# Optimization experiments

Measured on AMD Instinct MI355X. Metric: run time of the kernel, lower is better.

Reference implementation:

```python
import jax, jax.numpy as jnp
import numpy as np

B, S, D, H = 2, 2048, 1024, 16
DH = D // H
EPS = 1e-5


def setup_inputs() -> dict:
    key = jax.random.key(0)
    ks = jax.random.split(key, 12)
    inp = {
        "Q_source": jax.random.normal(ks[0], (B, S, D), jnp.float32),
        "K_source": jax.random.normal(ks[1], (B, S, D), jnp.float32),
        "V_source": jax.random.normal(ks[2], (B, S, D), jnp.float32),
        "padding_mask": jnp.zeros((B, 1, 1, S), dtype=bool),  # no padded keys (avoids NaN rows)
        "future_mask": jnp.triu(jnp.ones((S, S), dtype=bool), k=1)[None, None],  # causal
    }
    sc = 1.0 / np.sqrt(D)
    names = ["WQ", "WK", "WV", "WO"]
    for i, n in enumerate(names):
        inp[n] = jax.random.normal(ks[3 + i], (D, D), jnp.float32) * sc
        inp["b" + n[1]] = jnp.zeros((D,), jnp.float32)
    inp["gamma"] = jnp.ones((D,), jnp.float32)
    inp["beta"] = jnp.zeros((D,), jnp.float32)
    return inp


def reference(Q_source, K_source, V_source, padding_mask, future_mask,
              WQ, bQ, WK, bK, WV, bV, WO, bO, gamma, beta):
    b = Q_source.shape[0]
    # torch Linear: x @ W.T + b ; reshape to [B, H, S, DH]
    def proj(x, W, bb):
        y = x @ W.T + bb
        return y.reshape(b, -1, H, DH).transpose(0, 2, 1, 3)

    Q = proj(Q_source, WQ, bQ)
    K = proj(K_source, WK, bK)
    V = proj(V_source, WV, bV)

    scores = jnp.einsum("bhqd,bhkd->bhqk", Q, K) / jnp.sqrt(jnp.float32(DH))
    neg_inf = jnp.float32(-jnp.inf)
    scores = jnp.where(padding_mask, neg_inf, scores)
    scores = jnp.where(future_mask, neg_inf, scores)
    attn = jax.nn.softmax(scores, axis=-1)

    ctx = jnp.einsum("bhqk,bhkd->bhqd", attn, V)
    ctx = ctx.transpose(0, 2, 1, 3).reshape(b, -1, D)
    out = ctx @ WO.T + bO

    x = Q_source + out
    mu = x.mean(-1, keepdims=True)
    var = x.var(-1, keepdims=True)
    return (x - mu) * jax.lax.rsqrt(var + EPS) * gamma + beta
```

## Files before the change

### kernel.cpp

```cpp
#include <hip/hip_runtime.h>

#define S_LEN 2048
#define DMODEL 1024
#define NH 16
#define DHD 64

typedef __attribute__((ext_vector_type(8))) short bh8;
typedef __attribute__((ext_vector_type(4))) float f32x4;
typedef __attribute__((ext_vector_type(2))) unsigned int u32x2;
typedef __attribute__((ext_vector_type(4))) unsigned int u32x4;
typedef unsigned short u16;
typedef unsigned int u32;

static __device__ __forceinline__ u16 f2bf(float f) {
    unsigned u = __builtin_bit_cast(unsigned, f);
    u += 0x7fffu + ((u >> 16) & 1u);
    return (u16)(u >> 16);
}

typedef const __attribute__((address_space(1))) void* gptr_t;
typedef __attribute__((address_space(3))) void* lptr_t;

static __device__ __forceinline__ void gll16(const void* g, void* l) {
    __builtin_amdgcn_global_load_lds((gptr_t)g, (lptr_t)l, 16, 0, 0);
}

__global__ __launch_bounds__(256) void cvt_all(const float* __restrict__ WQ, const float* __restrict__ WK,
                                               const float* __restrict__ WV, const float* __restrict__ WO,
                                               const float* __restrict__ S0, const float* __restrict__ S1,
                                               const float* __restrict__ S2,
                                               u16* __restrict__ wq, u16* __restrict__ wk,
                                               u16* __restrict__ wv, u16* __restrict__ wo,
                                               u16* __restrict__ q0, u16* __restrict__ k0,
                                               u16* __restrict__ v0) {
    int bid = blockIdx.x;
    const float* s;
    u16* o;
    size_t base;
    if (bid < 2048) {
        int wi = bid >> 9;
        s = wi == 0 ? WQ : (wi == 1 ? WK : (wi == 2 ? WV : WO));
        o = wi == 0 ? wq : (wi == 1 ? wk : (wi == 2 ? wv : wo));
        base = (size_t)(bid & 511) * 2048;
    } else {
        int r = bid - 2048;
        int si = r >> 11;
        s = si == 0 ? S0 : (si == 1 ? S1 : S2);
        o = si == 0 ? q0 : (si == 1 ? k0 : v0);
        base = (size_t)(r & 2047) * 2048;
    }
    size_t i = base + (size_t)threadIdx.x * 8;
    float4 a = *(const float4*)(s + i);
    float4 b = *(const float4*)(s + i + 4);
    u32 p0 = (u32)f2bf(a.x) | ((u32)f2bf(a.y) << 16);
    u32 p1 = (u32)f2bf(a.z) | ((u32)f2bf(a.w) << 16);
    u32 p2 = (u32)f2bf(b.x) | ((u32)f2bf(b.y) << 16);
    u32 p3 = (u32)f2bf(b.z) | ((u32)f2bf(b.w) << 16);
    *(u32x4*)(o + i) = (u32x4){p0, p1, p2, p3};
}

template <int BM, int OBF, int AF32>
static __device__ __forceinline__ void gemm_body(const void* __restrict__ Ap, const u16* __restrict__ Bm,
                                                 const float* __restrict__ bias, void* __restrict__ Cv,
                                                 int N, int K, int bi, int bj, short* Al, short* Bl,
                                                 float oscale) {
    constexpr int MI = BM / 32;
    constexpr int NC = BM / 64;
    int tid = threadIdx.x, lane = tid & 63, w = tid >> 6;
    int ln = lane & 15, hi = lane >> 4;
    int wm = w >> 1, wn = w & 1;
    f32x4 acc[MI][4];
#pragma unroll
    for (int i = 0; i < MI; i++)
#pragma unroll
        for (int j = 0; j < 4; j++) acc[i][j] = (f32x4){0.f, 0.f, 0.f, 0.f};
    int nk = K >> 5;

    float4 fa[NC][2];
    auto loadA = [&](int kt) {
#pragma unroll
        for (int c = 0; c < NC; ++c) {
            int o = c * 4096 + tid * 16;
            int row = o >> 6, e0 = (o & 63) >> 1;
            const float* src = (const float*)Ap + (size_t)(bi * BM + row) * K + kt * 32 + e0;
            fa[c][0] = *(const float4*)src;
            fa[c][1] = *(const float4*)(src + 4);
        }
    };
    auto writeA = [&](int buf) {
#pragma unroll
        for (int c = 0; c < NC; ++c) {
            int o = c * 4096 + tid * 16;
            u32 w0 = (u32)f2bf(fa[c][0].x) | ((u32)f2bf(fa[c][0].y) << 16);
            u32 w1 = (u32)f2bf(fa[c][0].z) | ((u32)f2bf(fa[c][0].w) << 16);
            u32 w2 = (u32)f2bf(fa[c][1].x) | ((u32)f2bf(fa[c][1].y) << 16);
            u32 w3 = (u32)f2bf(fa[c][1].z) | ((u32)f2bf(fa[c][1].w) << 16);
            *(u32x4*)((char*)(Al + buf * (BM * 32)) + o) = (u32x4){w0, w1, w2, w3};
        }
    };
    auto stageA_lds = [&](int buf, int kt) {
#pragma unroll
        for (int c = 0; c < NC; ++c) {
            int o = c * 4096 + tid * 16;
            int row = o >> 6, col = (o & 63) >> 1;
            gll16((const u16*)Ap + (size_t)(bi * BM + row) * K + kt * 32 + col,
                  (char*)(Al + buf * (BM * 32)) + o);
        }
    };
    auto stageB = [&](int buf, int kt) {
#pragma unroll
        for (int c = 0; c < 2; ++c) {
            int o = c * 4096 + tid * 16;
            int row = o >> 6, col = (o & 63) >> 1;
            gll16(Bm + (size_t)(bj * 128 + row) * K + kt * 32 + col, (char*)(Bl + buf * 4096) + o);
        }
    };

    if constexpr (AF32) { loadA(0); writeA(0); } else { stageA_lds(0, 0); }
    stageB(0, 0);
    __syncthreads();
    int cur = 0;
    for (int kt = 0; kt < nk; ++kt) {
        bool pre = (kt + 1 < nk);
        if (pre) {
            if constexpr (AF32) loadA(kt + 1); else stageA_lds(cur ^ 1, kt + 1);
            stageB(cur ^ 1, kt + 1);
        }
        bh8 av[MI], bv[4];
#pragma unroll
        for (int i = 0; i < MI; i++) av[i] = *(const bh8*)&Al[cur * (BM * 32) + (wm * (BM / 2) + i * 16 + ln) * 32 + hi * 8];
#pragma unroll
        for (int j = 0; j < 4; j++) bv[j] = *(const bh8*)&Bl[cur * 4096 + (wn * 64 + j * 16 + ln) * 32 + hi * 8];
#pragma unroll
        for (int i = 0; i < MI; i++)
#pragma unroll
            for (int j = 0; j < 4; j++)
                acc[i][j] = __builtin_amdgcn_mfma_f32_16x16x32_bf16(av[i], bv[j], acc[i][j], 0, 0, 0);
        if constexpr (AF32) { if (pre) writeA(cur ^ 1); }
        __syncthreads();
        cur ^= 1;
    }
    if constexpr (OBF == 2) {
#pragma unroll
        for (int j = 0; j < 4; j++) {
            int col = wn * 64 + j * 16 + ln;
            float bvs = bias[bj * 128 + col];
#pragma unroll
            for (int i = 0; i < MI; i++) {
                int row0 = wm * (BM / 2) + i * 16 + hi * 4;
                u32 p01 = (u32)f2bf(acc[i][j][0] + bvs) | ((u32)f2bf(acc[i][j][1] + bvs) << 16);
                u32 p23 = (u32)f2bf(acc[i][j][2] + bvs) | ((u32)f2bf(acc[i][j][3] + bvs) << 16);
                int idx = col * 128 + (row0 ^ ((col & 7) << 3));
                *(u32x2*)&Al[idx] = (u32x2){p01, p23};
            }
        }
        __syncthreads();
        int b = bi >> 4;
        int sbase = (bi & 15) * 128;
#pragma unroll
        for (int it = 0; it < 8; ++it) {
            int idx = it * 256 + tid;
            int dcol = idx >> 4;
            int sl = (idx & 15) * 8;
            bh8 v = *(const bh8*)&Al[dcol * 128 + (sl ^ ((dcol & 7) << 3))];
            int h = bj * 2 + (dcol >> 6), d = dcol & 63;
            *(bh8*)((u16*)Cv + ((size_t)((b * 16 + h) * 64 + d)) * 2048 + sbase + sl) = v;
        }
        return;
    }
#pragma unroll
    for (int j = 0; j < 4; j++) {
        int col = bj * 128 + wn * 64 + j * 16 + ln;
        float bvs = bias[col];
#pragma unroll
        for (int i = 0; i < MI; i++) {
            int row0 = bi * BM + wm * (BM / 2) + i * 16 + hi * 4;
#pragma unroll
            for (int rr = 0; rr < 4; rr++) {
                if (OBF) {
                    float v = (acc[i][j][rr] + bvs) * oscale;
                    ((u16*)Cv)[(size_t)(row0 + rr) * N + col] = f2bf(v);
                } else {
                    ((float*)Cv)[(size_t)(row0 + rr) * N + col] = acc[i][j][rr] + bvs;
                }
            }
        }
    }
}

__global__ __launch_bounds__(256, 3) void gemm_qkv(const u16* __restrict__ A0, const u16* __restrict__ A1,
                                                   const u16* __restrict__ A2, const u16* __restrict__ B0,
                                                   const u16* __restrict__ B1, const u16* __restrict__ B2,
                                                   const float* __restrict__ c0, const float* __restrict__ c1,
                                                   const float* __restrict__ c2, u16* __restrict__ C0,
                                                   u16* __restrict__ C1, u16* __restrict__ VT) {
    __shared__ short SH[16384];
    short* Al = SH;
    short* Bl = SH + 8192;
    int bid = blockIdx.x;
    int swz = (bid & 7) * 96 + (bid >> 3);
    int z = swz >> 8, t = swz & 255;
    if (z == 2) {
        gemm_body<128, 2, 0>(A2, B2, c2, VT, 1024, 1024, t >> 3, t & 7, Al, Bl, 1.0f);
    } else if (z == 0) {
        gemm_body<128, 1, 0>(A0, B0, c0, C0, 1024, 1024, t >> 3, t & 7, Al, Bl, 0.18033688f);
    } else {
        gemm_body<128, 1, 0>(A1, B1, c1, C1, 1024, 1024, t >> 3, t & 7, Al, Bl, 1.0f);
    }
}

__global__ __launch_bounds__(256) void gemm_o(const u16* __restrict__ A, const u16* __restrict__ Bm,
                                              const float* __restrict__ bias, float* __restrict__ C) {
    __shared__ short Al[2 * 64 * 32];
    __shared__ short Bl[2 * 128 * 32];
    int bid = blockIdx.x;
    int swz = (bid & 7) * 64 + (bid >> 3);
    gemm_body<64, 0, 0>(A, Bm, bias, C, 1024, 1024, swz >> 3, swz & 7, Al, Bl, 1.0f);
}

template <int PLO, int PHI>
static __device__ __forceinline__ void attn_core(const u16* __restrict__ Qp, const u16* __restrict__ Kp,
                                                 const u16* __restrict__ VT, u16* __restrict__ Ctx,
                                                 short* Klb, short* Vlb, short* Pw, float* Csh, float* Lsh,
                                                 int b, int h, int bh, int qt, int tid) {
    int lane = tid & 63, w = tid >> 6;
    int grp = w >> 2;
    int qsub = w & 3;
    int tgl = tid & 255;
    int ln = lane & 15, hi = lane >> 4;
    __builtin_amdgcn_s_setprio(PLO);

    auto stage_kv = [&](int buf, int kt) {
#pragma unroll
        for (int c = 0; c < 2; ++c) {
            int o = c * 4096 + tgl * 16;
            int rr = o >> 7;
            int slot = (o >> 4) & 7;
            gll16(Kp + ((size_t)(b * S_LEN + kt * 64 + rr)) * DMODEL + h * DHD + ((slot ^ (rr & 7)) << 3),
                  (char*)(Klb + buf * 4096) + o);
            gll16(VT + ((size_t)(bh * DHD + rr)) * S_LEN + kt * 64 + ((slot ^ (rr & 7)) << 3),
                  (char*)(Vlb + buf * 4096) + o);
        }
    };

    int nh = qt + 1;
    int nt = 2 * qt + 2;
    int kbase = grp * nh;
    int qg0 = (qt << 7) + qsub * 32 + ln;
    const bh8* qr0 = (const bh8*)(Qp + ((size_t)(b * S_LEN + qg0)) * DMODEL + h * DHD);
    const bh8* qr1 = (const bh8*)(Qp + ((size_t)(b * S_LEN + qg0 + 16)) * DMODEL + h * DHD);
    bh8 qf[2][2];
    qf[0][0] = qr0[hi]; qf[0][1] = qr0[4 + hi];
    qf[1][0] = qr1[hi]; qf[1][1] = qr1[4 + hi];
    f32x4 ctxa[2][4];
    float ls[2] = {0.f, 0.f};
#pragma unroll
    for (int g = 0; g < 2; g++)
#pragma unroll
        for (int i = 0; i < 4; i++) ctxa[g][i] = (f32x4){0.f, 0.f, 0.f, 0.f};
    stage_kv(0, kbase);
    __syncthreads();
    int cur = 0;
    for (int i = 0; i < nh; ++i) {
        int kt = kbase + i;
        if (i + 1 < nh) stage_kv(cur ^ 1, kt + 1);
        f32x4 sc[2][4];
#pragma unroll
        for (int g = 0; g < 2; g++)
#pragma unroll
            for (int ks = 0; ks < 4; ++ks) sc[g][ks] = (f32x4){0.f, 0.f, 0.f, 0.f};
        __builtin_amdgcn_s_setprio(PHI);
#pragma unroll
        for (int dwin = 0; dwin < 2; ++dwin) {
#pragma unroll
            for (int ks = 0; ks < 4; ++ks) {
                int rr = ks * 16 + ln;
                bh8 kv = *(const bh8*)&Klb[cur * 4096 + rr * 64 + ((dwin * 32 + hi * 8) ^ ((rr & 7) << 3))];
                sc[0][ks] = __builtin_amdgcn_mfma_f32_16x16x32_bf16(kv, qf[0][dwin], sc[0][ks], 0, 0, 0);
                sc[1][ks] = __builtin_amdgcn_mfma_f32_16x16x32_bf16(kv, qf[1][dwin], sc[1][ks], 0, 0, 0);
            }
        }
        __builtin_amdgcn_s_setprio(PLO);
        if (kt >= nt - 2) {
#pragma unroll
            for (int g = 0; g < 2; g++) {
                int qgq = qg0 + g * 16;
#pragma unroll
                for (int ks = 0; ks < 4; ++ks)
#pragma unroll
                    for (int rr = 0; rr < 4; ++rr) {
                        int kg = kt * 64 + ks * 16 + hi * 4 + rr;
                        sc[g][ks][rr] = (kg <= qgq) ? sc[g][ks][rr] : -1e30f;
                    }
            }
        }
#pragma unroll
        for (int g = 0; g < 2; g++) {
#pragma unroll
            for (int ks = 0; ks < 4; ++ks) {
                float p0 = __builtin_amdgcn_exp2f(sc[g][ks][0]);
                float p1 = __builtin_amdgcn_exp2f(sc[g][ks][1]);
                float p2 = __builtin_amdgcn_exp2f(sc[g][ks][2]);
                float p3 = __builtin_amdgcn_exp2f(sc[g][ks][3]);
                ls[g] += (p0 + p1) + (p2 + p3);
                u32 u0 = __builtin_bit_cast(u32, p0);
                u32 u1 = __builtin_bit_cast(u32, p1);
                u32 u2 = __builtin_bit_cast(u32, p2);
                u32 u3 = __builtin_bit_cast(u32, p3);
                u32 a01 = (u0 >> 16) | (u1 & 0xffff0000u);
                u32 a23 = (u2 >> 16) | (u3 & 0xffff0000u);
                int kloc = ks * 16 + hi * 4;
                *(u32x2*)&Pw[ln * 64 + (kloc ^ ((ln & 7) << 3))] = (u32x2){a01, a23};
            }
            __builtin_amdgcn_s_setprio(PHI);
#pragma unroll
            for (int kw = 0; kw < 2; ++kw) {
                bh8 pf = *(const bh8*)&Pw[ln * 64 + ((kw * 32 + hi * 8) ^ ((ln & 7) << 3))];
#pragma unroll
                for (int ds = 0; ds < 4; ++ds) {
                    int d = ds * 16 + ln;
                    bh8 vf = *(const bh8*)&Vlb[cur * 4096 + d * 64 + ((kw * 32 + hi * 8) ^ ((d & 7) << 3))];
                    ctxa[g][ds] = __builtin_amdgcn_mfma_f32_16x16x32_bf16(vf, pf, ctxa[g][ds], 0, 0, 0);
                }
            }
            __builtin_amdgcn_s_setprio(PLO);
        }
        __syncthreads();
        cur ^= 1;
    }
#pragma unroll
    for (int g = 0; g < 2; g++) {
        ls[g] += __shfl_xor(ls[g], 16);
        ls[g] += __shfl_xor(ls[g], 32);
    }
    __builtin_amdgcn_s_setprio(0);
    if (grp == 1) {
#pragma unroll
        for (int g = 0; g < 2; g++) {
            int qloc = g * 16 + ln;
#pragma unroll
            for (int ds = 0; ds < 4; ++ds) {
                int doff = (ds * 16 + hi * 4) ^ ((qloc & 7) << 3);
                *(f32x4*)&Csh[(qsub * 32 + qloc) * 64 + doff] = ctxa[g][ds];
            }
            if (hi == 0) Lsh[qsub * 32 + qloc] = ls[g];
        }
    }
    __syncthreads();
    if (grp == 0) {
#pragma unroll
        for (int g = 0; g < 2; g++) {
            int qloc = g * 16 + ln;
            float inv = 1.f / (ls[g] + Lsh[qsub * 32 + qloc]);
            u16* cp = Ctx + ((size_t)(b * S_LEN + qg0 + g * 16)) * DMODEL + h * DHD;
#pragma unroll
            for (int ds = 0; ds < 4; ++ds) {
                int doff = (ds * 16 + hi * 4) ^ ((qloc & 7) << 3);
                f32x4 p = *(const f32x4*)&Csh[(qsub * 32 + qloc) * 64 + doff];
                ushort4 st;
                st.x = f2bf((ctxa[g][ds][0] + p[0]) * inv);
                st.y = f2bf((ctxa[g][ds][1] + p[1]) * inv);
                st.z = f2bf((ctxa[g][ds][2] + p[2]) * inv);
                st.w = f2bf((ctxa[g][ds][3] + p[3]) * inv);
                *(ushort4*)(cp + ds * 16 + hi * 4) = st;
            }
        }
    }
}

__global__ __launch_bounds__(512, 4) void attn_fwd(const u16* __restrict__ Qp, const u16* __restrict__ Kp,
                                                   const u16* __restrict__ VT, u16* __restrict__ Ctx) {
    __shared__ short Kl[2][2][4096];
    __shared__ short Vl[2][2][4096];
    __shared__ short Pl[8][1024];
    int tid = threadIdx.x, w = tid >> 6;
    int grp = w >> 2;
    int bid = blockIdx.x;
    int xcd = bid & 7;
    int qt = 15 - (bid >> 5);
    int bh = xcd * 4 + ((bid >> 3) & 3);
    int b = bh >> 4, h = bh & 15;
    float* Csh = (float*)&Kl[0][0][0];
    float* Lsh = (float*)&Pl[4][0];
    if (qt >= 8)
        attn_core<2, 3>(Qp, Kp, VT, Ctx, &Kl[grp][0][0], &Vl[grp][0][0], &Pl[w][0], Csh, Lsh, b, h, bh, qt, tid);
    else
        attn_core<0, 1>(Qp, Kp, VT, Ctx, &Kl[grp][0][0], &Vl[grp][0][0], &Pl[w][0], Csh, Lsh, b, h, bh, qt, tid);
}

__global__ __launch_bounds__(256) void ln_res(const float* __restrict__ Xres, const float* __restrict__ Y,
                                              const float* __restrict__ gamma, const float* __restrict__ beta,
                                              float* __restrict__ out) {
    int row = blockIdx.x, tid = threadIdx.x;
    const float4* xr = (const float4*)(Xres + (size_t)row * DMODEL);
    const float4* yr = (const float4*)(Y + (size_t)row * DMODEL);
    float4 a = xr[tid], bq = yr[tid];
    float x0 = a.x + bq.x, x1 = a.y + bq.y, x2 = a.z + bq.z, x3 = a.w + bq.w;
    float s1 = x0 + x1 + x2 + x3;
    float s2 = x0 * x0 + x1 * x1 + x2 * x2 + x3 * x3;
#pragma unroll
    for (int off = 32; off > 0; off >>= 1) {
        s1 += __shfl_xor(s1, off);
        s2 += __shfl_xor(s2, off);
    }
    __shared__ float r1[4], r2[4];
    int wv = tid >> 6;
    if ((tid & 63) == 0) { r1[wv] = s1; r2[wv] = s2; }
    __syncthreads();
    s1 = r1[0] + r1[1] + r1[2] + r1[3];
    s2 = r2[0] + r2[1] + r2[2] + r2[3];
    float mu = s1 * (1.0f / 1024.0f);
    float var = s2 * (1.0f / 1024.0f) - mu * mu;
    float rstd = rsqrtf(var + 1e-5f);
    const float4* g4 = (const float4*)gamma;
    const float4* b4 = (const float4*)beta;
    float4 g = g4[tid], bb = b4[tid];
    float4 res;
    res.x = (x0 - mu) * rstd * g.x + bb.x;
    res.y = (x1 - mu) * rstd * g.y + bb.y;
    res.z = (x2 - mu) * rstd * g.z + bb.z;
    res.w = (x3 - mu) * rstd * g.w + bb.w;
    *((float4*)(out + (size_t)row * DMODEL) + tid) = res;
}

extern "C" void kernel_launch(void* const* d_in, const int* in_sizes, int n_in,
                              void* d_out, int out_size, void* d_ws, size_t ws_size,
                              hipStream_t stream) {
    const float* Qs = (const float*)d_in[0];
    const float* Ks = (const float*)d_in[1];
    const float* Vs = (const float*)d_in[2];
    const float* WQ = (const float*)d_in[5];
    const float* bQ = (const float*)d_in[6];
    const float* WK = (const float*)d_in[7];
    const float* bK = (const float*)d_in[8];
    const float* WV = (const float*)d_in[9];
    const float* bV = (const float*)d_in[10];
    const float* WO = (const float*)d_in[11];
    const float* bO = (const float*)d_in[12];
    const float* gamma = (const float*)d_in[13];
    const float* beta = (const float*)d_in[14];

    const size_t MB = 1u << 20;
    char* w8 = (char*)d_ws;
    u16* Qb  = (u16*)(w8 + 0 * MB);
    u16* Kb  = (u16*)(w8 + 8 * MB);
    u16* Vb  = (u16*)(w8 + 16 * MB);
    u16* WQb = (u16*)(w8 + 24 * MB);
    u16* WKb = (u16*)(w8 + 26 * MB);
    u16* WVb = (u16*)(w8 + 28 * MB);
    u16* WOb = (u16*)(w8 + 30 * MB);
    u16* Qp  = (u16*)(w8 + 32 * MB);
    u16* Kp  = (u16*)(w8 + 40 * MB);
    u16* VTb = (u16*)(w8 + 56 * MB);
    u16* Ctx = (u16*)(w8 + 64 * MB);
    float* Y2 = (float*)(w8 + 72 * MB);

    cvt_all<<<8192, 256, 0, stream>>>(WQ, WK, WV, WO, Qs, Ks, Vs, WQb, WKb, WVb, WOb, Qb, Kb, Vb);
    gemm_qkv<<<768, 256, 0, stream>>>(Qb, Kb, Vb, WQb, WKb, WVb, bQ, bK, bV, Qp, Kp, VTb);
    attn_fwd<<<512, 512, 0, stream>>>(Qp, Kp, VTb, Ctx);
    gemm_o<<<512, 256, 0, stream>>>(Ctx, WOb, bO, Y2);
    ln_res<<<4096, 256, 0, stream>>>(Qs, Y2, gamma, beta, (float*)d_out);
}
```

Measured before the change: 117.9 us.

## Load K/V straight into registers and shrink attention blocks to two waves

```diff
diff --git a/kernel.cpp b/kernel.cpp
--- a/kernel.cpp
+++ b/kernel.cpp
@@ -221,49 +221,49 @@
 template <int PLO, int PHI>
 static __device__ __forceinline__ void attn_core(const u16* __restrict__ Qp, const u16* __restrict__ Kp,
                                                  const u16* __restrict__ VT, u16* __restrict__ Ctx,
-                                                 short* Klb, short* Vlb, short* Pw, float* Csh, float* Lsh,
-                                                 int b, int h, int bh, int qt, int tid) {
-    int lane = tid & 63, w = tid >> 6;
-    int grp = w >> 2;
-    int qsub = w & 3;
-    int tgl = tid & 255;
+                                                 short* Pw, int b, int h, int bh, int qt, int w, int lane) {
     int ln = lane & 15, hi = lane >> 4;
     __builtin_amdgcn_s_setprio(PLO);
-
-    auto stage_kv = [&](int buf, int kt) {
-#pragma unroll
-        for (int c = 0; c < 2; ++c) {
-            int o = c * 4096 + tgl * 16;
-            int rr = o >> 7;
-            int slot = (o >> 4) & 7;
-            gll16(Kp + ((size_t)(b * S_LEN + kt * 64 + rr)) * DMODEL + h * DHD + ((slot ^ (rr & 7)) << 3),
-                  (char*)(Klb + buf * 4096) + o);
-            gll16(VT + ((size_t)(bh * DHD + rr)) * S_LEN + kt * 64 + ((slot ^ (rr & 7)) << 3),
-                  (char*)(Vlb + buf * 4096) + o);
-        }
-    };
-
-    int nh = qt + 1;
-    int nt = 2 * qt + 2;
-    int kbase = grp * nh;
-    int qg0 = (qt << 7) + qsub * 32 + ln;
+    int nt = qt + 1;
+    int qg0 = (qt << 6) + w * 32 + ln;
     const bh8* qr0 = (const bh8*)(Qp + ((size_t)(b * S_LEN + qg0)) * DMODEL + h * DHD);
     const bh8* qr1 = (const bh8*)(Qp + ((size_t)(b * S_LEN + qg0 + 16)) * DMODEL + h * DHD);
     bh8 qf[2][2];
     qf[0][0] = qr0[hi]; qf[0][1] = qr0[4 + hi];
     qf[1][0] = qr1[hi]; qf[1][1] = qr1[4 + hi];
+
+    const u16* kp0 = Kp + ((size_t)(b * S_LEN + ln)) * DMODEL + h * DHD + hi * 8;
+    const u16* vp0 = VT + ((size_t)(bh * DHD + ln)) * S_LEN + hi * 8;
+
+    bh8 kr[4][2], vr[4][2];
+    auto loadK = [&](int kt) {
+        const u16* p = kp0 + (size_t)kt * 64 * DMODEL;
+#pragma unroll
+        for (int ks = 0; ks < 4; ++ks) {
+            kr[ks][0] = *(const bh8*)(p + (size_t)ks * 16 * DMODEL);
+            kr[ks][1] = *(const bh8*)(p + (size_t)ks * 16 * DMODEL + 32);
+        }
+    };
+    auto loadV = [&](int kt) {
+        const u16* p = vp0 + kt * 64;
+#pragma unroll
+        for (int ds = 0; ds < 4; ++ds) {
+            vr[ds][0] = *(const bh8*)(p + (size_t)ds * 16 * S_LEN);
+            vr[ds][1] = *(const bh8*)(p + (size_t)ds * 16 * S_LEN + 32);
+        }
+    };
+
     f32x4 ctxa[2][4];
     float ls[2] = {0.f, 0.f};
 #pragma unroll
     for (int g = 0; g < 2; g++)
 #pragma unroll
         for (int i = 0; i < 4; i++) ctxa[g][i] = (f32x4){0.f, 0.f, 0.f, 0.f};
-    stage_kv(0, kbase);
-    __syncthreads();
-    int cur = 0;
-    for (int i = 0; i < nh; ++i) {
-        int kt = kbase + i;
-        if (i + 1 < nh) stage_kv(cur ^ 1, kt + 1);
+
+    loadK(0);
+    loadV(0);
+    for (int kt = 0; kt < nt; ++kt) {
+        bool pre = (kt + 1 < nt);
         f32x4 sc[2][4];
 #pragma unroll
         for (int g = 0; g < 2; g++)
@@ -274,14 +274,13 @@
         for (int dwin = 0; dwin < 2; ++dwin) {
 #pragma unroll
             for (int ks = 0; ks < 4; ++ks) {
-                int rr = ks * 16 + ln;
-                bh8 kv = *(const bh8*)&Klb[cur * 4096 + rr * 64 + ((dwin * 32 + hi * 8) ^ ((rr & 7) << 3))];
-                sc[0][ks] = __builtin_amdgcn_mfma_f32_16x16x32_bf16(kv, qf[0][dwin], sc[0][ks], 0, 0, 0);
-                sc[1][ks] = __builtin_amdgcn_mfma_f32_16x16x32_bf16(kv, qf[1][dwin], sc[1][ks], 0, 0, 0);
+                sc[0][ks] = __builtin_amdgcn_mfma_f32_16x16x32_bf16(kr[ks][dwin], qf[0][dwin], sc[0][ks], 0, 0, 0);
+                sc[1][ks] = __builtin_amdgcn_mfma_f32_16x16x32_bf16(kr[ks][dwin], qf[1][dwin], sc[1][ks], 0, 0, 0);
             }
         }
         __builtin_amdgcn_s_setprio(PLO);
-        if (kt >= nt - 2) {
+        if (pre) loadK(kt + 1);
+        if (kt == nt - 1) {
 #pragma unroll
             for (int g = 0; g < 2; g++) {
                 int qgq = qg0 + g * 16;
@@ -317,16 +316,12 @@
             for (int kw = 0; kw < 2; ++kw) {
                 bh8 pf = *(const bh8*)&Pw[ln * 64 + ((kw * 32 + hi * 8) ^ ((ln & 7) << 3))];
 #pragma unroll
-                for (int ds = 0; ds < 4; ++ds) {
-                    int d = ds * 16 + ln;
-                    bh8 vf = *(const bh8*)&Vlb[cur * 4096 + d * 64 + ((kw * 32 + hi * 8) ^ ((d & 7) << 3))];
-                    ctxa[g][ds] = __builtin_amdgcn_mfma_f32_16x16x32_bf16(vf, pf, ctxa[g][ds], 0, 0, 0);
-                }
+                for (int ds = 0; ds < 4; ++ds)
+                    ctxa[g][ds] = __builtin_amdgcn_mfma_f32_16x16x32_bf16(vr[ds][kw], pf, ctxa[g][ds], 0, 0, 0);
             }
             __builtin_amdgcn_s_setprio(PLO);
         }
-        __syncthreads();
-        cur ^= 1;
+        if (pre) loadV(kt + 1);
     }
 #pragma unroll
     for (int g = 0; g < 2; g++) {
@@ -334,58 +329,35 @@
         ls[g] += __shfl_xor(ls[g], 32);
     }
     __builtin_amdgcn_s_setprio(0);
-    if (grp == 1) {
-#pragma unroll
-        for (int g = 0; g < 2; g++) {
-            int qloc = g * 16 + ln;
-#pragma unroll
-            for (int ds = 0; ds < 4; ++ds) {
-                int doff = (ds * 16 + hi * 4) ^ ((qloc & 7) << 3);
-                *(f32x4*)&Csh[(qsub * 32 + qloc) * 64 + doff] = ctxa[g][ds];
-            }
-            if (hi == 0) Lsh[qsub * 32 + qloc] = ls[g];
-        }
-    }
-    __syncthreads();
-    if (grp == 0) {
-#pragma unroll
-        for (int g = 0; g < 2; g++) {
-            int qloc = g * 16 + ln;
-            float inv = 1.f / (ls[g] + Lsh[qsub * 32 + qloc]);
-            u16* cp = Ctx + ((size_t)(b * S_LEN + qg0 + g * 16)) * DMODEL + h * DHD;
-#pragma unroll
-            for (int ds = 0; ds < 4; ++ds) {
-                int doff = (ds * 16 + hi * 4) ^ ((qloc & 7) << 3);
-                f32x4 p = *(const f32x4*)&Csh[(qsub * 32 + qloc) * 64 + doff];
-                ushort4 st;
-                st.x = f2bf((ctxa[g][ds][0] + p[0]) * inv);
-                st.y = f2bf((ctxa[g][ds][1] + p[1]) * inv);
-                st.z = f2bf((ctxa[g][ds][2] + p[2]) * inv);
-                st.w = f2bf((ctxa[g][ds][3] + p[3]) * inv);
-                *(ushort4*)(cp + ds * 16 + hi * 4) = st;
-            }
-        }
-    }
-}
-
-__global__ __launch_bounds__(512, 4) void attn_fwd(const u16* __restrict__ Qp, const u16* __restrict__ Kp,
+#pragma unroll
+    for (int g = 0; g < 2; g++) {
+        float inv = 1.f / ls[g];
+        u16* cp = Ctx + ((size_t)(b * S_LEN + qg0 + g * 16)) * DMODEL + h * DHD;
+#pragma unroll
+        for (int ds = 0; ds < 4; ++ds) {
+            ushort4 st;
+            st.x = f2bf(ctxa[g][ds][0] * inv);
+            st.y = f2bf(ctxa[g][ds][1] * inv);
+            st.z = f2bf(ctxa[g][ds][2] * inv);
+            st.w = f2bf(ctxa[g][ds][3] * inv);
+            *(ushort4*)(cp + ds * 16 + hi * 4) = st;
+        }
+    }
+}
+
+__global__ __launch_bounds__(128, 2) void attn_fwd(const u16* __restrict__ Qp, const u16* __restrict__ Kp,
                                                    const u16* __restrict__ VT, u16* __restrict__ Ctx) {
-    __shared__ short Kl[2][2][4096];
-    __shared__ short Vl[2][2][4096];
-    __shared__ short Pl[8][1024];
-    int tid = threadIdx.x, w = tid >> 6;
-    int grp = w >> 2;
+    __shared__ short Pl[2][1024];
+    int tid = threadIdx.x, lane = tid & 63, w = tid >> 6;
     int bid = blockIdx.x;
     int xcd = bid & 7;
-    int qt = 15 - (bid >> 5);
     int bh = xcd * 4 + ((bid >> 3) & 3);
+    int qt = 31 - (bid >> 5);
     int b = bh >> 4, h = bh & 15;
-    float* Csh = (float*)&Kl[0][0][0];
-    float* Lsh = (float*)&Pl[4][0];
-    if (qt >= 8)
-        attn_core<2, 3>(Qp, Kp, VT, Ctx, &Kl[grp][0][0], &Vl[grp][0][0], &Pl[w][0], Csh, Lsh, b, h, bh, qt, tid);
+    if (qt >= 16)
+        attn_core<2, 3>(Qp, Kp, VT, Ctx, &Pl[w][0], b, h, bh, qt, w, lane);
     else
-        attn_core<0, 1>(Qp, Kp, VT, Ctx, &Kl[grp][0][0], &Vl[grp][0][0], &Pl[w][0], Csh, Lsh, b, h, bh, qt, tid);
+        attn_core<0, 1>(Qp, Kp, VT, Ctx, &Pl[w][0], b, h, bh, qt, w, lane);
 }
 
 __global__ __launch_bounds__(256) void ln_res(const float* __restrict__ Xres, const float* __restrict__ Y,
@@ -457,7 +429,7 @@
 
     cvt_all<<<8192, 256, 0, stream>>>(WQ, WK, WV, WO, Qs, Ks, Vs, WQb, WKb, WVb, WOb, Qb, Kb, Vb);
     gemm_qkv<<<768, 256, 0, stream>>>(Qb, Kb, Vb, WQb, WKb, WVb, bQ, bK, bV, Qp, Kp, VTb);
-    attn_fwd<<<512, 512, 0, stream>>>(Qp, Kp, VTb, Ctx);
+    attn_fwd<<<1024, 128, 0, stream>>>(Qp, Kp, VTb, Ctx);
     gemm_o<<<512, 256, 0, stream>>>(Ctx, WOb, bO, Y2);
     ln_res<<<4096, 256, 0, stream>>>(Qs, Y2, gamma, beta, (float*)d_out);
 }
```

After: 153.7 us. 30.4% more time.
